# Performance work log

Hardware: AMD Instinct MI355X
Metric: run time of the kernel (lower is better)

## Reference

```python
import jax, jax.numpy as jnp
import numpy as np

N_NODES = 100000
N_EDGES = 1600000
IN_CH = 128
OUT_CH = 64
NEG_SLOPE = 0.2
EPS = 1e-10


def setup_inputs() -> dict:
    key = jax.random.key(0)
    k1, k2, k3, k4, k5 = jax.random.split(key, 5)
    x = jax.random.normal(k1, (N_NODES, IN_CH), dtype=jnp.float32)
    edge_index = jax.random.randint(k2, (2, N_EDGES), 0, N_NODES, dtype=jnp.int64)
    W = jax.random.normal(k3, (OUT_CH, IN_CH), dtype=jnp.float32) * (1.0 / np.sqrt(IN_CH))
    a_l = jax.random.normal(k4, (OUT_CH,), dtype=jnp.float32) * (1.0 / np.sqrt(OUT_CH))
    a_r = jax.random.normal(k5, (OUT_CH,), dtype=jnp.float32) * (1.0 / np.sqrt(OUT_CH))
    bias = jnp.zeros((OUT_CH,), dtype=jnp.float32)
    return {"x": x, "edge_index": edge_index, "W": W, "a_l": a_l, "a_r": a_r, "bias": bias}


def reference(x, edge_index, W, a_l, a_r, bias):
    N = x.shape[0]
    h = x @ W.T                     # (N, out_ch)
    src, dst = edge_index[0], edge_index[1]
    e_l = h @ a_l                   # (N,)
    e_r = h @ a_r                   # (N,)
    edge_attn = jax.nn.leaky_relu(e_l[dst] + e_r[src], negative_slope=NEG_SLOPE)  # (E,)
    # segment softmax over incoming edges of each dst node
    edge_max = jax.ops.segment_max(edge_attn, dst, num_segments=N)  # (N,), -inf for isolated
    edge_attn = jnp.exp(edge_attn - edge_max[dst])
    edge_sum = jax.ops.segment_sum(edge_attn, dst, num_segments=N)  # (N,)
    edge_attn = edge_attn / (edge_sum[dst] + EPS)
    messages = h[src] * edge_attn[:, None]                          # (E, out_ch)
    out = jax.ops.segment_sum(messages, dst, num_segments=N)        # (N, out_ch)
    return out + bias
```

## Files before the change

kernel.cpp:

```cpp
#include <hip/hip_runtime.h>
#include <math.h>

#define NN 100000
#define NE 1600000
#define IC 128
#define OC 64
#define NEG_SLOPE 0.2f
#define EPS_F 1e-10f

#define NSLICE 500
#define SN 200
#define EB 500
#define QPB 800
#define EPB 3200
#define CAPSEG 3600

typedef short bf16x8 __attribute__((ext_vector_type(8)));
typedef float f32x4 __attribute__((ext_vector_type(4)));

__device__ __forceinline__ unsigned short f2bf(float f) {
    unsigned u = __float_as_uint(f);
    u += 0x7fff + ((u >> 16) & 1);
    return (unsigned short)(u >> 16);
}

__global__ __launch_bounds__(256) void linear_kernel(
    const float* __restrict__ x, const float* __restrict__ W,
    const float* __restrict__ a_l, const float* __restrict__ a_r,
    unsigned short* __restrict__ h_bf, float* __restrict__ e_l,
    float* __restrict__ e_r, int* __restrict__ gcur)
{
    __shared__ unsigned short lds[128 * 136];
    const int tid = threadIdx.x;
    const int n0 = blockIdx.x * 64;

    if (blockIdx.x == 0) {
        for (int i = tid; i < NSLICE; i += 256) gcur[i] = 0;
    }

#pragma unroll
    for (int it = 0; it < 8; it++) {
        int i = it * 256 + tid;
        int r = i >> 5, c4 = i & 31;
        int n = n0 + r;
        float4 v = make_float4(0.f, 0.f, 0.f, 0.f);
        if (n < NN) v = *(const float4*)&x[(size_t)n * 128 + (c4 << 2)];
        ushort4 b;
        b.x = f2bf(v.x); b.y = f2bf(v.y); b.z = f2bf(v.z); b.w = f2bf(v.w);
        *(ushort4*)&lds[r * 136 + (c4 << 2)] = b;
    }
#pragma unroll
    for (int it = 0; it < 8; it++) {
        int i = it * 256 + tid;
        int r = i >> 5, c4 = i & 31;
        float4 v = *(const float4*)&W[r * 128 + (c4 << 2)];
        ushort4 b;
        b.x = f2bf(v.x); b.y = f2bf(v.y); b.z = f2bf(v.z); b.w = f2bf(v.w);
        *(ushort4*)&lds[(64 + r) * 136 + (c4 << 2)] = b;
    }
    __syncthreads();

    const int wv = tid >> 6;
    const int lane = tid & 63;
    const int q = lane >> 4;
    const int c = lane & 15;

    f32x4 acc[4];
#pragma unroll
    for (int t = 0; t < 4; t++) acc[t] = (f32x4){0.f, 0.f, 0.f, 0.f};

    const unsigned short* xrow = &lds[(wv * 16 + c) * 136];
    const unsigned short* wrow = &lds[(64 + c) * 136];

#pragma unroll
    for (int kk = 0; kk < 4; kk++) {
        int ko = kk * 32 + q * 8;
        bf16x8 a = *(const bf16x8*)&xrow[ko];
#pragma unroll
        for (int t = 0; t < 4; t++) {
            bf16x8 b = *(const bf16x8*)&wrow[t * 16 * 136 + ko];
            acc[t] = __builtin_amdgcn_mfma_f32_16x16x32_bf16(a, b, acc[t], 0, 0, 0);
        }
    }

#pragma unroll
    for (int r = 0; r < 4; r++) {
        int m = n0 + wv * 16 + q * 4 + r;
        if (m < NN) {
#pragma unroll
            for (int t = 0; t < 4; t++)
                h_bf[(size_t)m * OC + t * 16 + c] = f2bf(acc[t][r]);
        }
    }

    float al[4], ar[4];
#pragma unroll
    for (int t = 0; t < 4; t++) { al[t] = a_l[t * 16 + c]; ar[t] = a_r[t * 16 + c]; }
    float pl[4], pr[4];
#pragma unroll
    for (int r = 0; r < 4; r++) {
        pl[r] = al[0] * acc[0][r] + al[1] * acc[1][r] + al[2] * acc[2][r] + al[3] * acc[3][r];
        pr[r] = ar[0] * acc[0][r] + ar[1] * acc[1][r] + ar[2] * acc[2][r] + ar[3] * acc[3][r];
    }
#pragma unroll
    for (int m = 1; m < 16; m <<= 1) {
#pragma unroll
        for (int r = 0; r < 4; r++) {
            pl[r] += __shfl_xor(pl[r], m);
            pr[r] += __shfl_xor(pr[r], m);
        }
    }
    if (c == 0) {
#pragma unroll
        for (int r = 0; r < 4; r++) {
            int m = n0 + wv * 16 + q * 4 + r;
            if (m < NN) { e_l[m] = pl[r]; e_r[m] = pr[r]; }
        }
    }
}

__global__ __launch_bounds__(256) void bucket2_kernel(
    const int* __restrict__ src, const int* __restrict__ dst,
    int* __restrict__ gcur, int* __restrict__ bucketed)
{
    __shared__ int hist[NSLICE];
    __shared__ int base[NSLICE];
    __shared__ int lcur[NSLICE];
    __shared__ int gp[EPB];
    __shared__ int pay[EPB];
    __shared__ int wsums[4];

    const int t = threadIdx.x, b = blockIdx.x;
    for (int i = t; i < NSLICE; i += 256) hist[i] = 0;
    __syncthreads();

    for (int qi = t; qi < QPB; qi += 256) {
        int4 d = ((const int4*)dst)[b * QPB + qi];
        atomicAdd(&hist[d.x / SN], 1);
        atomicAdd(&hist[d.y / SN], 1);
        atomicAdd(&hist[d.z / SN], 1);
        atomicAdd(&hist[d.w / SN], 1);
    }
    __syncthreads();

    const int lane = t & 63, w4 = t >> 6;
    int a0 = (2 * t < NSLICE) ? hist[2 * t] : 0;
    int a1 = (2 * t + 1 < NSLICE) ? hist[2 * t + 1] : 0;
    int pairsum = a0 + a1;
    int incl = pairsum;
#pragma unroll
    for (int o = 1; o < 64; o <<= 1) {
        int u = __shfl_up(incl, o);
        if (lane >= o) incl += u;
    }
    if (lane == 63) wsums[w4] = incl;
    __syncthreads();
    if (t == 0) {
        int run = 0;
#pragma unroll
        for (int k = 0; k < 4; k++) { int x = wsums[k]; wsums[k] = run; run += x; }
    }
    __syncthreads();
    int excl = incl - pairsum + wsums[w4];
    if (2 * t < NSLICE) {
        int s0 = 2 * t;
        base[s0] = s0 * CAPSEG + atomicAdd(&gcur[s0], a0);
        hist[s0] = excl;
        lcur[s0] = excl;
    }
    if (2 * t + 1 < NSLICE) {
        int s1 = 2 * t + 1;
        base[s1] = s1 * CAPSEG + atomicAdd(&gcur[s1], a1);
        hist[s1] = excl + a0;
        lcur[s1] = excl + a0;
    }
    __syncthreads();

    for (int qi = t; qi < QPB; qi += 256) {
        int4 d4 = ((const int4*)dst)[b * QPB + qi];
        int4 s4 = ((const int4*)src)[b * QPB + qi];
        int dd[4] = {d4.x, d4.y, d4.z, d4.w};
        int ss[4] = {s4.x, s4.y, s4.z, s4.w};
#pragma unroll
        for (int k = 0; k < 4; k++) {
            int sl = dd[k] / SN;
            int slot = atomicAdd(&lcur[sl], 1);
            int gpos = base[sl] + (slot - hist[sl]);
            if (gpos - sl * CAPSEG >= CAPSEG) gpos = -1;
            gp[slot] = gpos;
            pay[slot] = ((dd[k] - sl * SN) << 17) | ss[k];
        }
    }
    __syncthreads();

    for (int i = t; i < EPB; i += 256) {
        int gpos = gp[i];
        if (gpos >= 0) bucketed[gpos] = pay[i];
    }
}

__global__ __launch_bounds__(1024, 8) void fused_sort_agg_kernel(
    const int* __restrict__ bucketed, const int* __restrict__ gcur,
    const float* __restrict__ e_l, const float* __restrict__ e_r,
    const unsigned short* __restrict__ h_bf, const float* __restrict__ bias,
    float* __restrict__ out)
{
    __shared__ int2 sorted[CAPSEG];
    __shared__ int hist[SN];
    __shared__ float el[SN];
    __shared__ int wsums[4];

    const int s = blockIdx.x, t = threadIdx.x;
    const int B0 = s * CAPSEG;
    int cnt = gcur[s];
    if (cnt > CAPSEG) cnt = CAPSEG;

    if (t < SN) {
        hist[t] = 0;
        el[t] = e_l[s * SN + t];
    }
    __syncthreads();

    int pr[4]; float wr[4];
#pragma unroll
    for (int k = 0; k < 4; k++) {
        int i = t + k * 1024;
        if (i < cnt) {
            int p = __builtin_nontemporal_load(&bucketed[B0 + i]);
            int dloc = p >> 17;
            float a = el[dloc] + e_r[p & 0x1FFFF];
            a = (a > 0.f) ? a : NEG_SLOPE * a;
            float w = __expf(a);
            pr[k] = p; wr[k] = w;
            atomicAdd(&hist[dloc], 1);
        }
    }
    __syncthreads();

    const int lane = t & 63, w4 = t >> 6;
    int v = (t < SN) ? hist[t] : 0;
    int incl = v;
#pragma unroll
    for (int o = 1; o < 64; o <<= 1) {
        int u = __shfl_up(incl, o);
        if (lane >= o) incl += u;
    }
    if (w4 < 4 && lane == 63) wsums[w4] = incl;
    __syncthreads();
    if (t == 0) {
        int run = 0;
#pragma unroll
        for (int k = 0; k < 4; k++) { int x = wsums[k]; wsums[k] = run; run += x; }
    }
    __syncthreads();
    int excl = incl - v + ((w4 < 4) ? wsums[w4] : 0);
    if (t < SN) hist[t] = excl;
    __syncthreads();

#pragma unroll
    for (int k = 0; k < 4; k++) {
        int i = t + k * 1024;
        if (i < cnt) {
            int dloc = pr[k] >> 17;
            int pos = atomicAdd(&hist[dloc], 1);
            sorted[pos] = make_int2(pr[k] & 0x1FFFF, __float_as_int(wr[k]));
        }
    }
    __syncthreads();

    const int g = t >> 3;
    const int ch = (t & 7) * 8;
    float4 bb0 = *(const float4*)&bias[ch];
    float4 bb1 = *(const float4*)&bias[ch + 4];

    for (int n = g; n < SN; n += 128) {
        const int start = (n == 0) ? 0 : hist[n - 1];
        const int end = hist[n];
        float acc[8] = {0.f, 0.f, 0.f, 0.f, 0.f, 0.f, 0.f, 0.f};
        float ws = 0.f;

        for (int j = start; j < end; j += 4) {
            int2 pp[4];
#pragma unroll
            for (int u = 0; u < 4; u++) {
                int e = j + u;
                pp[u] = sorted[(e < end) ? e : (end - 1)];
            }
            uint4 qq[4];
#pragma unroll
            for (int u = 0; u < 4; u++)
                qq[u] = *(const uint4*)(h_bf + (((unsigned)pp[u].x << 6) + ch));
#pragma unroll
            for (int u = 0; u < 4; u++) {
                float w = (j + u < end) ? __int_as_float(pp[u].y) : 0.f;
                ws += w;
                acc[0] += w * __uint_as_float(qq[u].x << 16);
                acc[1] += w * __uint_as_float(qq[u].x & 0xffff0000u);
                acc[2] += w * __uint_as_float(qq[u].y << 16);
                acc[3] += w * __uint_as_float(qq[u].y & 0xffff0000u);
                acc[4] += w * __uint_as_float(qq[u].z << 16);
                acc[5] += w * __uint_as_float(qq[u].z & 0xffff0000u);
                acc[6] += w * __uint_as_float(qq[u].w << 16);
                acc[7] += w * __uint_as_float(qq[u].w & 0xffff0000u);
            }
        }

        float rinv = 1.0f / (ws + EPS_F);
        int node = s * SN + n;
        f32x4 o0 = { acc[0] * rinv + bb0.x, acc[1] * rinv + bb0.y,
                     acc[2] * rinv + bb0.z, acc[3] * rinv + bb0.w };
        f32x4 o1 = { acc[4] * rinv + bb1.x, acc[5] * rinv + bb1.y,
                     acc[6] * rinv + bb1.z, acc[7] * rinv + bb1.w };
        __builtin_nontemporal_store(o0, (f32x4*)&out[(size_t)node * OC + ch]);
        __builtin_nontemporal_store(o1, (f32x4*)&out[(size_t)node * OC + ch + 4]);
    }
}

extern "C" void kernel_launch(void* const* d_in, const int* in_sizes, int n_in,
                              void* d_out, int out_size, void* d_ws, size_t ws_size,
                              hipStream_t stream)
{
    const float* x = (const float*)d_in[0];
    const int* edge_index = (const int*)d_in[1];
    const float* W = (const float*)d_in[2];
    const float* a_l = (const float*)d_in[3];
    const float* a_r = (const float*)d_in[4];
    const float* bias = (const float*)d_in[5];
    float* out = (float*)d_out;

    const int* src = edge_index;
    const int* dst = edge_index + NE;

    char* w = (char*)d_ws;
    unsigned short* h_bf = (unsigned short*)w;
    size_t off = (size_t)NN * OC * 2;
    float* e_l = (float*)(w + off); off += (size_t)NN * 4;
    float* e_r = (float*)(w + off); off += (size_t)NN * 4;
    int* gcur = (int*)(w + off);    off += (size_t)512 * 4;
    int* bucketed = (int*)(w + off); off += (size_t)NSLICE * CAPSEG * 4;

    linear_kernel<<<(NN + 63) / 64, 256, 0, stream>>>(x, W, a_l, a_r, h_bf, e_l, e_r, gcur);
    bucket2_kernel<<<EB, 256, 0, stream>>>(src, dst, gcur, bucketed);
    fused_sort_agg_kernel<<<NSLICE, 1024, 0, stream>>>(bucketed, gcur, e_l, e_r,
                                                       h_bf, bias, out);
}
```

Before: 174.5 us.

## Replace two-level slice bucketing with per-node fixed-capacity adjacency via global atomics

The two-stage slice bucketing and in-LDS counting sort are replaced by a scatter kernel. It claims a slot per edge with a global atomicAdd on a per-destination counter and writes the source id into a fixed 64-entry row for that node. A per-node aggregation kernel then reads each row contiguously and computes the attention weights inline. The goal is to drop the histogram, prefix-scan and LDS sort work and the large per-slice LDS footprint. The cost is 1.6M scattered global atomics and writes, and any edge beyond 64 per destination is silently dropped.

```diff
diff --git a/kernel.cpp b/kernel.cpp
--- a/kernel.cpp
+++ b/kernel.cpp
@@ -8,12 +8,8 @@
 #define NEG_SLOPE 0.2f
 #define EPS_F 1e-10f
 
-#define NSLICE 500
-#define SN 200
-#define EB 500
-#define QPB 800
-#define EPB 3200
-#define CAPSEG 3600
+#define CAPN 64
+#define NQ (NE / 4)
 
 typedef short bf16x8 __attribute__((ext_vector_type(8)));
 typedef float f32x4 __attribute__((ext_vector_type(4)));
@@ -28,14 +24,15 @@
     const float* __restrict__ x, const float* __restrict__ W,
     const float* __restrict__ a_l, const float* __restrict__ a_r,
     unsigned short* __restrict__ h_bf, float* __restrict__ e_l,
-    float* __restrict__ e_r, int* __restrict__ gcur)
+    float* __restrict__ e_r, int* __restrict__ cnt)
 {
     __shared__ unsigned short lds[128 * 136];
     const int tid = threadIdx.x;
     const int n0 = blockIdx.x * 64;
 
-    if (blockIdx.x == 0) {
-        for (int i = tid; i < NSLICE; i += 256) gcur[i] = 0;
+    {
+        int i = blockIdx.x * 256 + tid;
+        if (i < NN) cnt[i] = 0;
     }
 
 #pragma unroll
@@ -119,201 +116,80 @@
     }
 }
 
-__global__ __launch_bounds__(256) void bucket2_kernel(
+__global__ __launch_bounds__(256) void scatter_kernel(
     const int* __restrict__ src, const int* __restrict__ dst,
-    int* __restrict__ gcur, int* __restrict__ bucketed)
-{
-    __shared__ int hist[NSLICE];
-    __shared__ int base[NSLICE];
-    __shared__ int lcur[NSLICE];
-    __shared__ int gp[EPB];
-    __shared__ int pay[EPB];
-    __shared__ int wsums[4];
-
-    const int t = threadIdx.x, b = blockIdx.x;
-    for (int i = t; i < NSLICE; i += 256) hist[i] = 0;
-    __syncthreads();
-
-    for (int qi = t; qi < QPB; qi += 256) {
-        int4 d = ((const int4*)dst)[b * QPB + qi];
-        atomicAdd(&hist[d.x / SN], 1);
-        atomicAdd(&hist[d.y / SN], 1);
-        atomicAdd(&hist[d.z / SN], 1);
-        atomicAdd(&hist[d.w / SN], 1);
-    }
-    __syncthreads();
-
-    const int lane = t & 63, w4 = t >> 6;
-    int a0 = (2 * t < NSLICE) ? hist[2 * t] : 0;
-    int a1 = (2 * t + 1 < NSLICE) ? hist[2 * t + 1] : 0;
-    int pairsum = a0 + a1;
-    int incl = pairsum;
-#pragma unroll
-    for (int o = 1; o < 64; o <<= 1) {
-        int u = __shfl_up(incl, o);
-        if (lane >= o) incl += u;
-    }
-    if (lane == 63) wsums[w4] = incl;
-    __syncthreads();
-    if (t == 0) {
-        int run = 0;
-#pragma unroll
-        for (int k = 0; k < 4; k++) { int x = wsums[k]; wsums[k] = run; run += x; }
-    }
-    __syncthreads();
-    int excl = incl - pairsum + wsums[w4];
-    if (2 * t < NSLICE) {
-        int s0 = 2 * t;
-        base[s0] = s0 * CAPSEG + atomicAdd(&gcur[s0], a0);
-        hist[s0] = excl;
-        lcur[s0] = excl;
-    }
-    if (2 * t + 1 < NSLICE) {
-        int s1 = 2 * t + 1;
-        base[s1] = s1 * CAPSEG + atomicAdd(&gcur[s1], a1);
-        hist[s1] = excl + a0;
-        lcur[s1] = excl + a0;
-    }
-    __syncthreads();
-
-    for (int qi = t; qi < QPB; qi += 256) {
-        int4 d4 = ((const int4*)dst)[b * QPB + qi];
-        int4 s4 = ((const int4*)src)[b * QPB + qi];
-        int dd[4] = {d4.x, d4.y, d4.z, d4.w};
-        int ss[4] = {s4.x, s4.y, s4.z, s4.w};
-#pragma unroll
-        for (int k = 0; k < 4; k++) {
-            int sl = dd[k] / SN;
-            int slot = atomicAdd(&lcur[sl], 1);
-            int gpos = base[sl] + (slot - hist[sl]);
-            if (gpos - sl * CAPSEG >= CAPSEG) gpos = -1;
-            gp[slot] = gpos;
-            pay[slot] = ((dd[k] - sl * SN) << 17) | ss[k];
-        }
-    }
-    __syncthreads();
-
-    for (int i = t; i < EPB; i += 256) {
-        int gpos = gp[i];
-        if (gpos >= 0) bucketed[gpos] = pay[i];
-    }
-}
-
-__global__ __launch_bounds__(1024, 8) void fused_sort_agg_kernel(
-    const int* __restrict__ bucketed, const int* __restrict__ gcur,
+    int* __restrict__ cnt, int* __restrict__ seg)
+{
+    int qi = blockIdx.x * 256 + threadIdx.x;
+    if (qi >= NQ) return;
+    int4 d4 = ((const int4*)dst)[qi];
+    int4 s4 = ((const int4*)src)[qi];
+    int dd[4] = {d4.x, d4.y, d4.z, d4.w};
+    int ss[4] = {s4.x, s4.y, s4.z, s4.w};
+#pragma unroll
+    for (int k = 0; k < 4; k++) {
+        int pos = atomicAdd(&cnt[dd[k]], 1);
+        if (pos < CAPN) seg[dd[k] * CAPN + pos] = ss[k];
+    }
+}
+
+__global__ __launch_bounds__(256) void node_agg_kernel(
+    const int* __restrict__ cnt, const int* __restrict__ seg,
     const float* __restrict__ e_l, const float* __restrict__ e_r,
     const unsigned short* __restrict__ h_bf, const float* __restrict__ bias,
     float* __restrict__ out)
 {
-    __shared__ int2 sorted[CAPSEG];
-    __shared__ int hist[SN];
-    __shared__ float el[SN];
-    __shared__ int wsums[4];
-
-    const int s = blockIdx.x, t = threadIdx.x;
-    const int B0 = s * CAPSEG;
-    int cnt = gcur[s];
-    if (cnt > CAPSEG) cnt = CAPSEG;
-
-    if (t < SN) {
-        hist[t] = 0;
-        el[t] = e_l[s * SN + t];
-    }
-    __syncthreads();
-
-    int pr[4]; float wr[4];
-#pragma unroll
-    for (int k = 0; k < 4; k++) {
-        int i = t + k * 1024;
-        if (i < cnt) {
-            int p = __builtin_nontemporal_load(&bucketed[B0 + i]);
-            int dloc = p >> 17;
-            float a = el[dloc] + e_r[p & 0x1FFFF];
-            a = (a > 0.f) ? a : NEG_SLOPE * a;
-            float w = __expf(a);
-            pr[k] = p; wr[k] = w;
-            atomicAdd(&hist[dloc], 1);
-        }
-    }
-    __syncthreads();
-
-    const int lane = t & 63, w4 = t >> 6;
-    int v = (t < SN) ? hist[t] : 0;
-    int incl = v;
-#pragma unroll
-    for (int o = 1; o < 64; o <<= 1) {
-        int u = __shfl_up(incl, o);
-        if (lane >= o) incl += u;
-    }
-    if (w4 < 4 && lane == 63) wsums[w4] = incl;
-    __syncthreads();
-    if (t == 0) {
-        int run = 0;
-#pragma unroll
-        for (int k = 0; k < 4; k++) { int x = wsums[k]; wsums[k] = run; run += x; }
-    }
-    __syncthreads();
-    int excl = incl - v + ((w4 < 4) ? wsums[w4] : 0);
-    if (t < SN) hist[t] = excl;
-    __syncthreads();
-
-#pragma unroll
-    for (int k = 0; k < 4; k++) {
-        int i = t + k * 1024;
-        if (i < cnt) {
-            int dloc = pr[k] >> 17;
-            int pos = atomicAdd(&hist[dloc], 1);
-            sorted[pos] = make_int2(pr[k] & 0x1FFFF, __float_as_int(wr[k]));
-        }
-    }
-    __syncthreads();
-
+    const int t = threadIdx.x;
     const int g = t >> 3;
     const int ch = (t & 7) * 8;
+    const int n = blockIdx.x * 32 + g;
+
+    int deg = cnt[n];
+    if (deg > CAPN) deg = CAPN;
+    const float eln = e_l[n];
+    const int* segn = seg + n * CAPN;
     float4 bb0 = *(const float4*)&bias[ch];
     float4 bb1 = *(const float4*)&bias[ch + 4];
 
-    for (int n = g; n < SN; n += 128) {
-        const int start = (n == 0) ? 0 : hist[n - 1];
-        const int end = hist[n];
-        float acc[8] = {0.f, 0.f, 0.f, 0.f, 0.f, 0.f, 0.f, 0.f};
-        float ws = 0.f;
-
-        for (int j = start; j < end; j += 4) {
-            int2 pp[4];
-#pragma unroll
-            for (int u = 0; u < 4; u++) {
-                int e = j + u;
-                pp[u] = sorted[(e < end) ? e : (end - 1)];
-            }
-            uint4 qq[4];
-#pragma unroll
-            for (int u = 0; u < 4; u++)
-                qq[u] = *(const uint4*)(h_bf + (((unsigned)pp[u].x << 6) + ch));
-#pragma unroll
-            for (int u = 0; u < 4; u++) {
-                float w = (j + u < end) ? __int_as_float(pp[u].y) : 0.f;
-                ws += w;
-                acc[0] += w * __uint_as_float(qq[u].x << 16);
-                acc[1] += w * __uint_as_float(qq[u].x & 0xffff0000u);
-                acc[2] += w * __uint_as_float(qq[u].y << 16);
-                acc[3] += w * __uint_as_float(qq[u].y & 0xffff0000u);
-                acc[4] += w * __uint_as_float(qq[u].z << 16);
-                acc[5] += w * __uint_as_float(qq[u].z & 0xffff0000u);
-                acc[6] += w * __uint_as_float(qq[u].w << 16);
-                acc[7] += w * __uint_as_float(qq[u].w & 0xffff0000u);
-            }
-        }
-
-        float rinv = 1.0f / (ws + EPS_F);
-        int node = s * SN + n;
-        f32x4 o0 = { acc[0] * rinv + bb0.x, acc[1] * rinv + bb0.y,
-                     acc[2] * rinv + bb0.z, acc[3] * rinv + bb0.w };
-        f32x4 o1 = { acc[4] * rinv + bb1.x, acc[5] * rinv + bb1.y,
-                     acc[6] * rinv + bb1.z, acc[7] * rinv + bb1.w };
-        __builtin_nontemporal_store(o0, (f32x4*)&out[(size_t)node * OC + ch]);
-        __builtin_nontemporal_store(o1, (f32x4*)&out[(size_t)node * OC + ch + 4]);
-    }
+    float acc[8] = {0.f, 0.f, 0.f, 0.f, 0.f, 0.f, 0.f, 0.f};
+    float ws = 0.f;
+
+    for (int j = 0; j < deg; j += 4) {
+        int4 s4 = *(const int4*)(segn + j);
+        int ss[4] = {s4.x, s4.y, s4.z, s4.w};
+        int sv[4]; float er[4]; uint4 qq[4];
+#pragma unroll
+        for (int u = 0; u < 4; u++)
+            sv[u] = (j + u < deg) ? ss[u] : ss[0];
+#pragma unroll
+        for (int u = 0; u < 4; u++) er[u] = e_r[sv[u]];
+#pragma unroll
+        for (int u = 0; u < 4; u++)
+            qq[u] = *(const uint4*)(h_bf + (((unsigned)sv[u]) << 6) + ch);
+#pragma unroll
+        for (int u = 0; u < 4; u++) {
+            float a = eln + er[u];
+            a = (a > 0.f) ? a : NEG_SLOPE * a;
+            float w = (j + u < deg) ? __expf(a) : 0.f;
+            ws += w;
+            acc[0] += w * __uint_as_float(qq[u].x << 16);
+            acc[1] += w * __uint_as_float(qq[u].x & 0xffff0000u);
+            acc[2] += w * __uint_as_float(qq[u].y << 16);
+            acc[3] += w * __uint_as_float(qq[u].y & 0xffff0000u);
+            acc[4] += w * __uint_as_float(qq[u].z << 16);
+            acc[5] += w * __uint_as_float(qq[u].z & 0xffff0000u);
+            acc[6] += w * __uint_as_float(qq[u].w << 16);
+            acc[7] += w * __uint_as_float(qq[u].w & 0xffff0000u);
+        }
+    }
+
+    float rinv = 1.0f / (ws + EPS_F);
+    f32x4 o0 = { acc[0] * rinv + bb0.x, acc[1] * rinv + bb0.y,
+                 acc[2] * rinv + bb0.z, acc[3] * rinv + bb0.w };
+    f32x4 o1 = { acc[4] * rinv + bb1.x, acc[5] * rinv + bb1.y,
+                 acc[6] * rinv + bb1.z, acc[7] * rinv + bb1.w };
+    __builtin_nontemporal_store(o0, (f32x4*)&out[(size_t)n * OC + ch]);
+    __builtin_nontemporal_store(o1, (f32x4*)&out[(size_t)n * OC + ch + 4]);
 }
 
 extern "C" void kernel_launch(void* const* d_in, const int* in_sizes, int n_in,
@@ -336,11 +212,10 @@
     size_t off = (size_t)NN * OC * 2;
     float* e_l = (float*)(w + off); off += (size_t)NN * 4;
     float* e_r = (float*)(w + off); off += (size_t)NN * 4;
-    int* gcur = (int*)(w + off);    off += (size_t)512 * 4;
-    int* bucketed = (int*)(w + off); off += (size_t)NSLICE * CAPSEG * 4;
-
-    linear_kernel<<<(NN + 63) / 64, 256, 0, stream>>>(x, W, a_l, a_r, h_bf, e_l, e_r, gcur);
-    bucket2_kernel<<<EB, 256, 0, stream>>>(src, dst, gcur, bucketed);
-    fused_sort_agg_kernel<<<NSLICE, 1024, 0, stream>>>(bucketed, gcur, e_l, e_r,
-                                                       h_bf, bias, out);
-}
+    int* cnt = (int*)(w + off);     off += (size_t)NN * 4;
+    int* seg = (int*)(w + off);     off += (size_t)NN * CAPN * 4;
+
+    linear_kernel<<<(NN + 63) / 64, 256, 0, stream>>>(x, W, a_l, a_r, h_bf, e_l, e_r, cnt);
+    scatter_kernel<<<(NQ + 255) / 256, 256, 0, stream>>>(src, dst, cnt, seg);
+    node_agg_kernel<<<NN / 32, 256, 0, stream>>>(cnt, seg, e_l, e_r, h_bf, bias, out);
+}
```

Measured after the change: 278.8 us. 59.8% more time.
